# Kernel optimization log

Hardware: AMD Instinct MI355X
Metric: run time of the kernel (lower is better)

Reference implementation:

```python
import jax, jax.numpy as jnp
import numpy as np

N_BONDS = 16777216
N_ATOMS = 1048576
N_TYPES = 16


def setup_inputs() -> dict:
    key = jax.random.key(0)
    k1, k2, k3, k4, k5, k6 = jax.random.split(key, 6)
    # bond orders kept strictly positive so BO**p_be2 and its grad are finite
    bo_sigma = jax.random.uniform(k1, (N_BONDS,), jnp.float32, 0.05, 1.0)
    bo_pi = jax.random.uniform(k2, (N_BONDS,), jnp.float32, 0.05, 1.0)
    bo_pipi = jax.random.uniform(k3, (N_BONDS,), jnp.float32, 0.05, 1.0)
    bond_type = jax.random.randint(k4, (N_BONDS,), 0, N_TYPES, jnp.int32)
    atom_i = jax.random.randint(k5, (N_BONDS,), 0, N_ATOMS, jnp.int32)
    # columns: De_sigma, De_pi, De_pipi, p_be1, p_be2 (positive, O(1))
    bond_params = jax.random.uniform(k6, (N_TYPES, 5), jnp.float32, 0.1, 1.0)
    return {
        "bond_type": bond_type,
        "atom_i": atom_i,
        "bo_sigma": bo_sigma,
        "bo_pi": bo_pi,
        "bo_pipi": bo_pipi,
        "bond_params": bond_params,
        "n_atoms": N_ATOMS,
    }


def reference(bond_type, atom_i, bo_sigma, bo_pi, bo_pipi, bond_params, n_atoms):
    # Gather per-bond-type parameters: [E, 5]
    p = bond_params[bond_type]
    de_s, de_p, de_pp, p_be1, p_be2 = (p[:, 0], p[:, 1], p[:, 2], p[:, 3], p[:, 4])
    # ReaxFF bond energy per bond
    e_bond = (-de_s * bo_sigma * jnp.exp(p_be1 * (1.0 - bo_sigma ** p_be2))
              - de_p * bo_pi
              - de_pp * bo_pipi)
    # Scatter-reduce to per-atom energy
    e_atom = jax.ops.segment_sum(e_bond, atom_i, num_segments=n_atoms)
    return e_atom
```

## Files before the change

### kernel.cpp

```cpp
#include <hip/hip_runtime.h>


typedef float f32x4 __attribute__((ext_vector_type(4)));
typedef int   i32x4 __attribute__((ext_vector_type(4)));
typedef unsigned u32;
typedef unsigned short u16;

#define NB     512
#define RANGE  2048
#define SHIFT  11
#define TB     256
#define PADQ   8u

__device__ __forceinline__ u32 f32_to_bf16_bits(float f) {
    u32 u = __float_as_uint(f);
    return ((u + 0x7FFFu + ((u >> 16) & 1u)) >> 16) & 0xFFFFu;
}

__device__ __forceinline__ u32 block_excl_scan(u32 v, u32* wsum, int tid) {
    u32 s = v;
#pragma unroll
    for (int off = 1; off < 64; off <<= 1) {
        u32 n = __shfl_up(s, off);
        if ((tid & 63) >= off) s += n;
    }
    if ((tid & 63) == 63) wsum[tid >> 6] = s;
    __syncthreads();
    int w = tid >> 6;
    u32 wb = 0;
#pragma unroll
    for (int ww = 0; ww < 3; ++ww) wb += (ww < w) ? wsum[ww] : 0u;
    return wb + s - v;
}

template<int CBK>
__global__ __launch_bounds__(TB) void count_kernel(
        const i32x4* __restrict__ atom_i, u16* __restrict__ counts,
        int round_start) {
    __shared__ u32 hist[4][NB];
    int tid = threadIdx.x, w = tid >> 6;
    for (int i = tid; i < 4 * NB; i += TB) ((u32*)hist)[i] = 0u;
    __syncthreads();
    long base4 = ((long)round_start + (long)blockIdx.x * CBK) >> 2;
#pragma unroll
    for (int it = 0; it < CBK / (TB * 4); ++it) {
        i32x4 a = __builtin_nontemporal_load(&atom_i[base4 + it * TB + tid]);
        atomicAdd(&hist[w][(u32)a.x >> SHIFT], 1u);
        atomicAdd(&hist[w][(u32)a.y >> SHIFT], 1u);
        atomicAdd(&hist[w][(u32)a.z >> SHIFT], 1u);
        atomicAdd(&hist[w][(u32)a.w >> SHIFT], 1u);
    }
    __syncthreads();
    for (int b = tid; b < NB; b += TB)
        counts[(size_t)blockIdx.x * NB + b] =
            (u16)(hist[0][b] + hist[1][b] + hist[2][b] + hist[3][b]);
}

__global__ __launch_bounds__(TB) void scan_cols_kernel(
        const u16* __restrict__ counts, u32* __restrict__ offs,
        u32* __restrict__ total, int nsb) {
    __shared__ u32 sc[TB];
    int b = blockIdx.x, t = threadIdx.x;
    int vpt = nsb >> 8;
    u32 v[16];
    u32 s = 0;
    for (int k = 0; k < vpt; ++k) {
        u32 c = counts[(size_t)(t * vpt + k) * NB + b];
        c = (c + PADQ - 1u) & ~(PADQ - 1u);
        v[k] = s; s += c;
    }
    sc[t] = s;
    __syncthreads();
    for (int off = 1; off < TB; off <<= 1) {
        u32 u = (t >= off) ? sc[t - off] : 0u;
        __syncthreads();
        sc[t] += u;
        __syncthreads();
    }
    u32 excl = sc[t] - s;
    for (int k = 0; k < vpt; ++k)
        offs[(size_t)(t * vpt + k) * NB + b] = excl + v[k];
    if (t == TB - 1) total[b] = sc[t];
}

__global__ __launch_bounds__(TB) void base_kernel(
        const u32* __restrict__ total, u32* __restrict__ gbase) {
    __shared__ u32 wsum[4];
    int t = threadIdx.x;
    u32 t0 = total[2 * t], t1 = total[2 * t + 1];
    u32 excl = block_excl_scan(t0 + t1, wsum, t);
    gbase[2 * t]     = excl;
    gbase[2 * t + 1] = excl + t0;
}

template<int CBK, int MINB>
__global__ __launch_bounds__(TB, MINB) void partition_kernel(
        const i32x4* __restrict__ bt, const i32x4* __restrict__ ai,
        const f32x4* __restrict__ bs_, const f32x4* __restrict__ bp_,
        const f32x4* __restrict__ bpp_, const float* __restrict__ bond_params,
        const u16* __restrict__ counts, const u32* __restrict__ offs,
        const u32* __restrict__ gbase, u32* __restrict__ arena,
        int round_start) {
    __shared__ u32   sorted[CBK];
    __shared__ u32   start_[NB], cur[NB];
    __shared__ u32   wsum[4];
    __shared__ float4 sp_a[16];
    __shared__ float  sp_b[16];

    int tid = threadIdx.x, sb = blockIdx.x;
    if (tid < 16) {
        const float* p = bond_params + tid * 5;
        sp_a[tid] = make_float4(p[0], p[1], p[2], p[3]);
        sp_b[tid] = p[4];
    }
    u32 c01 = ((const u32*)(counts + (size_t)sb * NB))[tid];
    u32 c0 = c01 & 0xFFFFu, c1 = c01 >> 16;
    u32 excl = block_excl_scan(c0 + c1, wsum, tid);
    start_[2 * tid]     = excl;       cur[2 * tid]     = excl;
    start_[2 * tid + 1] = excl + c0;  cur[2 * tid + 1] = excl + c0;
    __syncthreads();

    long base4 = ((long)round_start + (long)sb * CBK) >> 2;
#pragma unroll
    for (int it = 0; it < CBK / (TB * 4); ++it) {
        long idx = base4 + it * TB + tid;
        i32x4 t  = __builtin_nontemporal_load(&bt[idx]);
        i32x4 a  = __builtin_nontemporal_load(&ai[idx]);
        f32x4 s  = __builtin_nontemporal_load(&bs_[idx]);
        f32x4 p  = __builtin_nontemporal_load(&bp_[idx]);
        f32x4 pp = __builtin_nontemporal_load(&bpp_[idx]);
#pragma unroll
        for (int k = 0; k < 4; ++k) {
            u32 ak = (u32)a[k];
            float4 pa = sp_a[t[k]];
            float  pb = sp_b[t[k]];
            float pw = __powf(s[k], pb);
            float e  = -pa.x * s[k] * __expf(pa.w * (1.0f - pw))
                       - pa.y * p[k] - pa.z * pp[k];
            u32 b = ak >> SHIFT;
            u32 pos = atomicAdd(&cur[b], 1u);
            sorted[pos] = ((ak & (RANGE - 1u)) << 16) | f32_to_bf16_bits(e);
        }
    }
    __syncthreads();

    constexpr int LG  = (CBK >= 8192) ? 16 : 8;
    constexpr int GPW = 64 / LG;
    int w = tid >> 6, lane = tid & 63;
    int gi = lane / LG, j0 = lane % LG;
    for (int b = w * GPW + gi; b < NB; b += 4 * GPW) {
        u32 end = cur[b], ls = start_[b], len = end - ls;
        u32 plen = (len + PADQ - 1u) & ~(PADQ - 1u);
        u32 g = gbase[b] + offs[(size_t)sb * NB + b];
        for (u32 j = j0; j < plen; j += LG)
            arena[g + j] = (j < len) ? sorted[ls + j] : 0u;
    }
}

__global__ __launch_bounds__(TB, 4) void accum_kernel(
        const u32* __restrict__ arena, const u32* __restrict__ total,
        const u32* __restrict__ gbase, float* __restrict__ out, int add_prev) {
    __shared__ float acc[4][RANGE];
    int tid = threadIdx.x, w = tid >> 6, b = blockIdx.x;
    for (int i = tid; i < RANGE; i += TB) {
        acc[0][i] = 0.f; acc[1][i] = 0.f; acc[2][i] = 0.f; acc[3][i] = 0.f;
    }
    __syncthreads();
    u32 s0 = gbase[b];
    u32 n  = total[b];
    const uint4* src = (const uint4*)(arena + s0);
    for (u32 j = tid; j < (n >> 2); j += TB) {
        uint4 e = src[j];
        if (e.x) atomicAdd(&acc[w][e.x >> 16], __uint_as_float((e.x & 0xFFFFu) << 16));
        if (e.y) atomicAdd(&acc[w][e.y >> 16], __uint_as_float((e.y & 0xFFFFu) << 16));
        if (e.z) atomicAdd(&acc[w][e.z >> 16], __uint_as_float((e.z & 0xFFFFu) << 16));
        if (e.w) atomicAdd(&acc[w][e.w >> 16], __uint_as_float((e.w & 0xFFFFu) << 16));
    }
    __syncthreads();
    size_t ob = (size_t)b * RANGE;
    for (int i = tid; i < RANGE; i += TB) {
        float v = acc[0][i] + acc[1][i] + acc[2][i] + acc[3][i];
        if (add_prev) v += out[ob + i];
        out[ob + i] = v;
    }
}

__global__ __launch_bounds__(TB) void zero_kernel(f32x4* __restrict__ p, int n4) {
    int i = blockIdx.x * blockDim.x + threadIdx.x;
    if (i < n4) p[i] = (f32x4)(0.f);
}

__global__ __launch_bounds__(TB) void atomic_fallback_kernel(
        const i32x4* __restrict__ bt, const i32x4* __restrict__ ai,
        const f32x4* __restrict__ bs_, const f32x4* __restrict__ bp_,
        const f32x4* __restrict__ bpp_, const float* __restrict__ bond_params,
        float* __restrict__ out, int n4) {
    __shared__ float sp[80];
    if (threadIdx.x < 80) sp[threadIdx.x] = bond_params[threadIdx.x];
    __syncthreads();
    int i = blockIdx.x * blockDim.x + threadIdx.x;
    if (i >= n4) return;
    i32x4 t  = bt[i]; i32x4 a = ai[i];
    f32x4 s  = bs_[i]; f32x4 p = bp_[i]; f32x4 pp = bpp_[i];
#pragma unroll
    for (int k = 0; k < 4; ++k) {
        const float* pr = sp + t[k] * 5;
        float pw = __powf(s[k], pr[4]);
        float e  = -pr[0] * s[k] * __expf(pr[3] * (1.0f - pw))
                   - pr[1] * p[k] - pr[2] * pp[k];
        unsafeAtomicAdd(&out[a[k]], e);
    }
}

extern "C" void kernel_launch(void* const* d_in, const int* in_sizes, int n_in,
                              void* d_out, int out_size, void* d_ws, size_t ws_size,
                              hipStream_t stream) {
    const int*   bond_type   = (const int*)  d_in[0];
    const int*   atom_i      = (const int*)  d_in[1];
    const float* bo_sigma    = (const float*)d_in[2];
    const float* bo_pi       = (const float*)d_in[3];
    const float* bo_pipi     = (const float*)d_in[4];
    const float* bond_params = (const float*)d_in[5];
    float*       e_atom      = (float*)d_out;

    const int n_bonds = in_sizes[0];
    const int n_atoms = out_size;

    int cfg_cb = 0, cfg_nr = 0;
    if (n_atoms == (NB << SHIFT)) {
        const int prefs[10][2] = {
            {4096, 1}, {4096, 2}, {8192, 1}, {8192, 2}, {4096, 4},
            {8192, 4}, {4096, 8}, {8192, 8}, {4096, 16}, {8192, 16}};
        for (int ci = 0; ci < 10 && !cfg_nr; ++ci) {
            int cb = prefs[ci][0], r = prefs[ci][1];
            if (n_bonds % (r * cb)) continue;
            long cpr = (long)n_bonds / r, nsb = cpr / cb;
            if (nsb % 256 || nsb < 256 || nsb > 4096) continue;
            size_t arena_worst = (size_t)cpr + (size_t)(PADQ - 1) * NB * nsb;
            size_t need = arena_worst * 4
                        + (size_t)nsb * NB * 4
                        + (size_t)NB * 4
                        + (size_t)NB * 4
                        + (size_t)nsb * NB * 2
                        + 256;
            if (need <= ws_size) { cfg_cb = cb; cfg_nr = r; }
        }
    }

    if (cfg_nr) {
        const int NR = cfg_nr, cpr = n_bonds / NR, nsb = cpr / cfg_cb;
        size_t arena_worst = (size_t)cpr + (size_t)(PADQ - 1) * NB * nsb;
        u32* arena  = (u32*)d_ws;
        u32* offs   = arena + arena_worst;
        u32* total  = offs + (size_t)nsb * NB;
        u32* gbase  = total + NB;
        u16* counts = (u16*)(gbase + NB);
        for (int r = 0; r < NR; ++r) {
            int rs = r * cpr;
            if (cfg_cb == 4096)
                count_kernel<4096><<<nsb, TB, 0, stream>>>(
                    (const i32x4*)atom_i, counts, rs);
            else
                count_kernel<8192><<<nsb, TB, 0, stream>>>(
                    (const i32x4*)atom_i, counts, rs);
            scan_cols_kernel<<<NB, TB, 0, stream>>>(counts, offs, total, nsb);
            base_kernel<<<1, TB, 0, stream>>>(total, gbase);
            if (cfg_cb == 4096)
                partition_kernel<4096, 7><<<nsb, TB, 0, stream>>>(
                    (const i32x4*)bond_type, (const i32x4*)atom_i,
                    (const f32x4*)bo_sigma, (const f32x4*)bo_pi,
                    (const f32x4*)bo_pipi, bond_params,
                    counts, offs, gbase, arena, rs);
            else
                partition_kernel<8192, 4><<<nsb, TB, 0, stream>>>(
                    (const i32x4*)bond_type, (const i32x4*)atom_i,
                    (const f32x4*)bo_sigma, (const f32x4*)bo_pi,
                    (const f32x4*)bo_pipi, bond_params,
                    counts, offs, gbase, arena, rs);
            accum_kernel<<<NB, TB, 0, stream>>>(arena, total, gbase, e_atom,
                                                r ? 1 : 0);
        }
    } else {
        int zn4 = n_atoms / 4;
        zero_kernel<<<(zn4 + TB - 1) / TB, TB, 0, stream>>>((f32x4*)e_atom, zn4);
        int n4 = n_bonds / 4;
        atomic_fallback_kernel<<<(n4 + TB - 1) / TB, TB, 0, stream>>>(
            (const i32x4*)bond_type, (const i32x4*)atom_i,
            (const f32x4*)bo_sigma, (const f32x4*)bo_pi, (const f32x4*)bo_pipi,
            bond_params, e_atom, n4);
    }
}
```

Measured before the change: 457.5 us.

## Prefetch partition loads, remap blocks, widen accum blocks, and prefer larger chunks

Several changes land together. The partition kernel software-prefetches the next iteration's inputs, drops the nontemporal hints, remaps block IDs across a stride of eight, and precomputes the global arena offsets into shared memory. The accum kernel now runs with 1024 threads per block. The config order prefers 8192-bond chunks, and the pad quantum and LG are raised to 16. Together these aim to hide load latency and raise memory parallelism, at the cost of more register pressure, extra arena padding and lower occupancy for the partition kernel.

New measurement: 446.8 us. 1.02x faster.

```diff
diff --git a/kernel.cpp b/kernel.cpp
--- a/kernel.cpp
+++ b/kernel.cpp
@@ -10,7 +10,7 @@
 #define RANGE  2048
 #define SHIFT  11
 #define TB     256
-#define PADQ   8u
+#define PADQ   16u
 
 __device__ __forceinline__ u32 f32_to_bf16_bits(float f) {
     u32 u = __float_as_uint(f);
@@ -44,7 +44,7 @@
     long base4 = ((long)round_start + (long)blockIdx.x * CBK) >> 2;
 #pragma unroll
     for (int it = 0; it < CBK / (TB * 4); ++it) {
-        i32x4 a = __builtin_nontemporal_load(&atom_i[base4 + it * TB + tid]);
+        i32x4 a = atom_i[base4 + it * TB + tid];
         atomicAdd(&hist[w][(u32)a.x >> SHIFT], 1u);
         atomicAdd(&hist[w][(u32)a.y >> SHIFT], 1u);
         atomicAdd(&hist[w][(u32)a.z >> SHIFT], 1u);
@@ -102,17 +102,22 @@
         const u32* __restrict__ gbase, u32* __restrict__ arena,
         int round_start) {
     __shared__ u32   sorted[CBK];
-    __shared__ u32   start_[NB], cur[NB];
+    __shared__ u32   start_[NB], cur[NB], gofs[NB];
     __shared__ u32   wsum[4];
     __shared__ float4 sp_a[16];
     __shared__ float  sp_b[16];
 
-    int tid = threadIdx.x, sb = blockIdx.x;
+    int tid = threadIdx.x;
+    int nsbK = gridDim.x, bid = blockIdx.x;
+    int sb = ((nsbK & 7) == 0) ? ((bid & 7) * (nsbK >> 3) + (bid >> 3)) : bid;
+
     if (tid < 16) {
         const float* p = bond_params + tid * 5;
         sp_a[tid] = make_float4(p[0], p[1], p[2], p[3]);
         sp_b[tid] = p[4];
     }
+    for (int b = tid; b < NB; b += TB)
+        gofs[b] = gbase[b] + offs[(size_t)sb * NB + b];
     u32 c01 = ((const u32*)(counts + (size_t)sb * NB))[tid];
     u32 c0 = c01 & 0xFFFFu, c1 = c01 >> 16;
     u32 excl = block_excl_scan(c0 + c1, wsum, tid);
@@ -120,56 +125,58 @@
     start_[2 * tid + 1] = excl + c0;  cur[2 * tid + 1] = excl + c0;
     __syncthreads();
 
+    constexpr int ITERS = CBK / (TB * 4);
     long base4 = ((long)round_start + (long)sb * CBK) >> 2;
-#pragma unroll
-    for (int it = 0; it < CBK / (TB * 4); ++it) {
-        long idx = base4 + it * TB + tid;
-        i32x4 t  = __builtin_nontemporal_load(&bt[idx]);
-        i32x4 a  = __builtin_nontemporal_load(&ai[idx]);
-        f32x4 s  = __builtin_nontemporal_load(&bs_[idx]);
-        f32x4 p  = __builtin_nontemporal_load(&bp_[idx]);
-        f32x4 pp = __builtin_nontemporal_load(&bpp_[idx]);
+    i32x4 tA = bt[base4 + tid], aA = ai[base4 + tid];
+    f32x4 sA = bs_[base4 + tid], pA = bp_[base4 + tid], ppA = bpp_[base4 + tid];
+#pragma unroll
+    for (int it = 0; it < ITERS; ++it) {
+        i32x4 tN, aN; f32x4 sN, pN, ppN;
+        if (it + 1 < ITERS) {
+            long nidx = base4 + (it + 1) * TB + tid;
+            tN = bt[nidx]; aN = ai[nidx];
+            sN = bs_[nidx]; pN = bp_[nidx]; ppN = bpp_[nidx];
+        }
 #pragma unroll
         for (int k = 0; k < 4; ++k) {
-            u32 ak = (u32)a[k];
-            float4 pa = sp_a[t[k]];
-            float  pb = sp_b[t[k]];
-            float pw = __powf(s[k], pb);
-            float e  = -pa.x * s[k] * __expf(pa.w * (1.0f - pw))
-                       - pa.y * p[k] - pa.z * pp[k];
+            u32 ak = (u32)aA[k];
+            float4 pa = sp_a[tA[k]];
+            float  pb = sp_b[tA[k]];
+            float pw = __powf(sA[k], pb);
+            float e  = -pa.x * sA[k] * __expf(pa.w * (1.0f - pw))
+                       - pa.y * pA[k] - pa.z * ppA[k];
             u32 b = ak >> SHIFT;
             u32 pos = atomicAdd(&cur[b], 1u);
             sorted[pos] = ((ak & (RANGE - 1u)) << 16) | f32_to_bf16_bits(e);
         }
-    }
-    __syncthreads();
-
-    constexpr int LG  = (CBK >= 8192) ? 16 : 8;
+        tA = tN; aA = aN; sA = sN; pA = pN; ppA = ppN;
+    }
+    __syncthreads();
+
+    constexpr int LG  = 16;
     constexpr int GPW = 64 / LG;
     int w = tid >> 6, lane = tid & 63;
     int gi = lane / LG, j0 = lane % LG;
     for (int b = w * GPW + gi; b < NB; b += 4 * GPW) {
         u32 end = cur[b], ls = start_[b], len = end - ls;
         u32 plen = (len + PADQ - 1u) & ~(PADQ - 1u);
-        u32 g = gbase[b] + offs[(size_t)sb * NB + b];
+        u32 g = gofs[b];
         for (u32 j = j0; j < plen; j += LG)
             arena[g + j] = (j < len) ? sorted[ls + j] : 0u;
     }
 }
 
-__global__ __launch_bounds__(TB, 4) void accum_kernel(
+__global__ __launch_bounds__(1024) void accum_kernel(
         const u32* __restrict__ arena, const u32* __restrict__ total,
         const u32* __restrict__ gbase, float* __restrict__ out, int add_prev) {
     __shared__ float acc[4][RANGE];
-    int tid = threadIdx.x, w = tid >> 6, b = blockIdx.x;
-    for (int i = tid; i < RANGE; i += TB) {
-        acc[0][i] = 0.f; acc[1][i] = 0.f; acc[2][i] = 0.f; acc[3][i] = 0.f;
-    }
+    int tid = threadIdx.x, w = (tid >> 6) & 3, b = blockIdx.x;
+    for (int i = tid; i < 4 * RANGE; i += 1024) ((float*)acc)[i] = 0.f;
     __syncthreads();
     u32 s0 = gbase[b];
     u32 n  = total[b];
     const uint4* src = (const uint4*)(arena + s0);
-    for (u32 j = tid; j < (n >> 2); j += TB) {
+    for (u32 j = tid; j < (n >> 2); j += 1024) {
         uint4 e = src[j];
         if (e.x) atomicAdd(&acc[w][e.x >> 16], __uint_as_float((e.x & 0xFFFFu) << 16));
         if (e.y) atomicAdd(&acc[w][e.y >> 16], __uint_as_float((e.y & 0xFFFFu) << 16));
@@ -178,7 +185,7 @@
     }
     __syncthreads();
     size_t ob = (size_t)b * RANGE;
-    for (int i = tid; i < RANGE; i += TB) {
+    for (int i = tid; i < RANGE; i += 1024) {
         float v = acc[0][i] + acc[1][i] + acc[2][i] + acc[3][i];
         if (add_prev) v += out[ob + i];
         out[ob + i] = v;
@@ -229,8 +236,8 @@
     int cfg_cb = 0, cfg_nr = 0;
     if (n_atoms == (NB << SHIFT)) {
         const int prefs[10][2] = {
-            {4096, 1}, {4096, 2}, {8192, 1}, {8192, 2}, {4096, 4},
-            {8192, 4}, {4096, 8}, {8192, 8}, {4096, 16}, {8192, 16}};
+            {8192, 1}, {4096, 1}, {8192, 2}, {4096, 2}, {8192, 4},
+            {4096, 4}, {8192, 8}, {4096, 8}, {8192, 16}, {4096, 16}};
         for (int ci = 0; ci < 10 && !cfg_nr; ++ci) {
             int cb = prefs[ci][0], r = prefs[ci][1];
             if (n_bonds % (r * cb)) continue;
@@ -266,7 +273,7 @@
             scan_cols_kernel<<<NB, TB, 0, stream>>>(counts, offs, total, nsb);
             base_kernel<<<1, TB, 0, stream>>>(total, gbase);
             if (cfg_cb == 4096)
-                partition_kernel<4096, 7><<<nsb, TB, 0, stream>>>(
+                partition_kernel<4096, 4><<<nsb, TB, 0, stream>>>(
                     (const i32x4*)bond_type, (const i32x4*)atom_i,
                     (const f32x4*)bo_sigma, (const f32x4*)bo_pi,
                     (const f32x4*)bo_pipi, bond_params,
@@ -277,8 +284,8 @@
                     (const f32x4*)bo_sigma, (const f32x4*)bo_pi,
                     (const f32x4*)bo_pipi, bond_params,
                     counts, offs, gbase, arena, rs);
-            accum_kernel<<<NB, TB, 0, stream>>>(arena, total, gbase, e_atom,
-                                                r ? 1 : 0);
+            accum_kernel<<<NB, 1024, 0, stream>>>(arena, total, gbase, e_atom,
+                                                  r ? 1 : 0);
         }
     } else {
         int zn4 = n_atoms / 4;
```
